# Optimization experiments

Measured on AMD Instinct MI355X. Metric: run time of the kernel, lower is better.

## Reference

```python
import jax, jax.numpy as jnp
import numpy as np

NSEG = 65  # instance ids live in [0, NSEG); must match setup_inputs fill_max
EPS = 1e-8


def setup_inputs() -> dict:
    key = jax.random.key(0)
    k1, k2 = jax.random.split(key)
    B, C, H, W = 8, 4, 1024, 1024
    logit = jax.random.normal(k1, (B, C, H, W), dtype=jnp.float32)
    inst_gt = jax.random.randint(k2, (B, H, W), 0, NSEG, dtype=jnp.int32)
    return {"logit": logit, "inst_gt": inst_gt}


def reference(logit, inst_gt):
    B, C, H, W = logit.shape
    N = H * W
    # softmax over channel dim (as F.softmax(logit, dim=1))
    p = jax.nn.softmax(logit, axis=1)                      # [B, C, H, W]
    p = p.reshape(B, C, N).transpose(0, 2, 1).reshape(B * N, C)  # [B*N, C]
    # one fused segment reduce over all batches: offset ids per batch element
    seg = (inst_gt.reshape(B, N) + jnp.arange(B, dtype=inst_gt.dtype)[:, None] * NSEG).reshape(-1)
    sums = jax.ops.segment_sum(p, seg, num_segments=B * NSEG)        # [B*NSEG, C]
    sumsq = jax.ops.segment_sum(p * p, seg, num_segments=B * NSEG)   # [B*NSEG, C]
    cnt = jax.ops.segment_sum(jnp.ones((B * N,), p.dtype), seg, num_segments=B * NSEG)  # [B*NSEG]
    cnt = cnt[:, None]                                               # [B*NSEG, 1]
    # unbiased variance per (batch, instance, channel): (sumsq - sum^2/n) / (n-1)
    n_safe = jnp.where(cnt > 0, cnt, 1.0)
    denom = jnp.where(cnt > 1, cnt - 1.0, 1.0)
    var = (sumsq - sums * sums / n_safe) / denom                     # [B*NSEG, C]
    var = var.reshape(B, NSEG, C)
    cnt = cnt.reshape(B, NSEG, 1)
    nonzero_id = (jnp.arange(NSEG) != 0)[None, :, None]              # skip background id 0
    # only instances with more than 1 pixel contribute variance
    valid = nonzero_id & (cnt > 1.0)
    sum_var = jnp.sum(jnp.where(valid, var, 0.0), axis=(1, 2))       # [B]
    # len(inst_ids): number of distinct nonzero ids present in each image
    num_ids = jnp.sum(jnp.where(nonzero_id[..., 0] & (cnt[..., 0] > 0.0), 1.0, 0.0), axis=1)  # [B]
    loss = jnp.mean(sum_var / (num_ids + EPS))
    return loss
```

## Files before the change

### kernel.cpp

```cpp
#include <hip/hip_runtime.h>


typedef unsigned int  uint32_t_;
typedef unsigned short u16x2 __attribute__((ext_vector_type(2)));
typedef unsigned int   u32x4 __attribute__((ext_vector_type(4)));
typedef short          s16x8 __attribute__((ext_vector_type(8)));
typedef float          f32x4 __attribute__((ext_vector_type(4)));

constexpr int   B_    = 8;
constexpr int   SEGS  = 64;
constexpr int   VALS  = 5;
constexpr float EPS_  = 1e-8f;

constexpr int PLANE   = 528;
constexpr int NSLOT   = 11;
constexpr int WLDS    = NSLOT * PLANE;
constexpr int LDS_SZ  = (4 * WLDS > 16384) ? 4 * WLDS : 16384;

__device__ __forceinline__ unsigned asu(float f)  { return __float_as_uint(f); }
__device__ __forceinline__ float    asf(unsigned u){ return __uint_as_float(u); }

__global__ __launch_bounds__(256) void vl_accum(const float* __restrict__ logit,
                                                const int*   __restrict__ inst,
                                                float* __restrict__ acc,
                                                int N, int ppb)
{
    __shared__ __align__(16) unsigned char lds[LDS_SZ];

    const int tid  = threadIdx.x;
    const int wid  = tid >> 6;
    const int lane = tid & 63;
    const int col  = lane & 15;
    const int quad = lane >> 4;
    const int wbase = wid * WLDS;

    *(uint2*)(lds + wbase + 8 * PLANE + lane * 8) = make_uint2(0x3F803F80u, 0x3F803F80u);
    *(uint2*)(lds + wbase + 9 * PLANE + lane * 8) = make_uint2(0u, 0u);

    int pl;
    if      (col < 4)              pl = col;
    else if (col >= 8 && col < 12) pl = col - 4;
    else if (col == 4)             pl = 8;
    else                           pl = 9;
    const int bRd   = wbase + pl * PLANE + quad * 16;
    const int segRd = wbase + 10 * PLANE + quad * 16;
    const int segWr = wbase + 10 * PLANE + lane * 8;

    u16x2 rowdup[4];
#pragma unroll
    for (int t = 0; t < 4; ++t) {
        unsigned short rw = (unsigned short)(t * 16 + col);
        rowdup[t] = (u16x2){rw, rw};
    }
    const u16x2 one2  = (u16x2){1, 1};
    const u16x2 bf1p  = (u16x2){0x3F80, 0x3F80};

    const int b = blockIdx.y;
    const float* __restrict__ l0 = logit + (size_t)b * 4 * N;
    const int*   __restrict__ ib = inst  + (size_t)b * N;

    f32x4 acc0 = {0.f,0.f,0.f,0.f}, acc1 = {0.f,0.f,0.f,0.f};
    f32x4 acc2 = {0.f,0.f,0.f,0.f}, acc3 = {0.f,0.f,0.f,0.f};

    const int blockStart = blockIdx.x * ppb;
    const int rounds = ppb >> 10;

    for (int r = 0; r < rounds; ++r) {
        const int q  = blockStart + (r << 10) + (wid << 8) + (lane << 2);
        const bool ok = (q + 4 <= N);
        const int qc = ok ? q : 0;

        float4 x0 = *(const float4*)(l0 + qc);
        float4 x1 = *(const float4*)(l0 + (size_t)N     + qc);
        float4 x2 = *(const float4*)(l0 + (size_t)2 * N + qc);
        float4 x3 = *(const float4*)(l0 + (size_t)3 * N + qc);
        int4   sg = *(const int4*)(ib + qc);
        if (!ok) sg = make_int4(0, 0, 0, 0);

        const float c0[4] = {x0.x, x0.y, x0.z, x0.w};
        const float c1[4] = {x1.x, x1.y, x1.z, x1.w};
        const float c2[4] = {x2.x, x2.y, x2.z, x2.w};
        const float c3[4] = {x3.x, x3.y, x3.z, x3.w};

        float P0[4], P1[4], P2[4], QQ[4];
#pragma unroll
        for (int i = 0; i < 4; ++i) {
            float va = c0[i], vb = c1[i], vc = c2[i], vd = c3[i];
            float m  = fmaxf(fmaxf(va, vb), fmaxf(vc, vd));
            float e0 = __expf(va - m);
            float e1 = __expf(vb - m);
            float e2 = __expf(vc - m);
            float e3 = __expf(vd - m);
            float rr = 1.0f / (e0 + e1 + e2 + e3);
            float q0 = e0 * rr, q1 = e1 * rr, q2 = e2 * rr, q3 = e3 * rr;
            P0[i] = q0; P1[i] = q1; P2[i] = q2;
            QQ[i] = q0*q0 + q1*q1 + q2*q2 + q3*q3;
        }

#define STAGE_PLANE(P, ARR)                                                     \
        {                                                                       \
            unsigned a0 = asu(ARR[0]), a1 = asu(ARR[1]);                        \
            unsigned a2 = asu(ARR[2]), a3 = asu(ARR[3]);                        \
            unsigned h1m = a1 & 0xFFFF0000u, h3m = a3 & 0xFFFF0000u;            \
            unsigned hi01 = (a0 >> 16) | h1m;                                   \
            unsigned hi23 = (a2 >> 16) | h3m;                                   \
            float l0f = ARR[0] - asf(a0 & 0xFFFF0000u);                         \
            float l1f = ARR[1] - asf(h1m);                                      \
            float l2f = ARR[2] - asf(a2 & 0xFFFF0000u);                         \
            float l3f = ARR[3] - asf(h3m);                                      \
            unsigned lo01 = (asu(l0f) >> 16) | (asu(l1f) & 0xFFFF0000u);        \
            unsigned lo23 = (asu(l2f) >> 16) | (asu(l3f) & 0xFFFF0000u);        \
            *(uint2*)(lds + wbase + (P) * PLANE + lane * 8)     = make_uint2(hi01, hi23); \
            *(uint2*)(lds + wbase + ((P)+4) * PLANE + lane * 8) = make_uint2(lo01, lo23); \
        }
        STAGE_PLANE(0, P0)
        STAGE_PLANE(1, P1)
        STAGE_PLANE(2, P2)
        STAGE_PLANE(3, QQ)
#undef STAGE_PLANE

        {
            unsigned r0 = (unsigned)(sg.x - 1) & 0xFFFFu;
            unsigned r1 = (unsigned)(sg.y - 1) & 0xFFFFu;
            unsigned r2 = (unsigned)(sg.z - 1) & 0xFFFFu;
            unsigned r3 = (unsigned)(sg.w - 1) & 0xFFFFu;
            *(uint2*)(lds + segWr) = make_uint2(r0 | (r1 << 16), r2 | (r3 << 16));
        }

#pragma unroll
        for (int kt = 0; kt < 8; ++kt) {
            s16x8 bfrag = *(const s16x8*)(lds + bRd   + kt * 64);
            u32x4 sv    = *(const u32x4*)(lds + segRd + kt * 64);

#define DO_TILE(T, ACC)                                                         \
            {                                                                   \
                u32x4 fr;                                                       \
                _Pragma("unroll")                                               \
                for (int i = 0; i < 4; ++i) {                                   \
                    u16x2 sp  = __builtin_bit_cast(u16x2, sv[i]);               \
                    u16x2 d   = sp - rowdup[T];                                 \
                    u16x2 mn  = __builtin_elementwise_min(d, one2);             \
                    u16x2 inv = one2 - mn;                                      \
                    u16x2 f   = inv * bf1p;                                     \
                    fr[i] = __builtin_bit_cast(unsigned, f);                    \
                }                                                               \
                s16x8 afrag = __builtin_bit_cast(s16x8, fr);                    \
                ACC = __builtin_amdgcn_mfma_f32_16x16x32_bf16(afrag, bfrag, ACC, 0, 0, 0); \
            }
            DO_TILE(0, acc0)
            DO_TILE(1, acc1)
            DO_TILE(2, acc2)
            DO_TILE(3, acc3)
#undef DO_TILE
        }
    }

    __syncthreads();
    float* cl = (float*)lds;
    {
        const int base = ((wid * 4) * 64 + lane) * 4;
        *(f32x4*)(cl + base)            = acc0;
        *(f32x4*)(cl + base + 64 * 4)   = acc1;
        *(f32x4*)(cl + base + 128 * 4)  = acc2;
        *(f32x4*)(cl + base + 192 * 4)  = acc3;
    }
    __syncthreads();

    for (int i = tid; i < SEGS * VALS; i += 256) {
        const int row = i / VALS;
        const int cc  = i - row * VALS;
        const int t   = row >> 4;
        const int rr  = row & 15;
        const int g   = rr >> 2;
        const int reg = rr & 3;
        const int lhi = g * 16 + cc;
        const int llo = lhi + 8;
        float v = 0.0f;
#pragma unroll
        for (int w = 0; w < 4; ++w) {
            v += cl[((w * 4 + t) * 64 + lhi) * 4 + reg];
            v += cl[((w * 4 + t) * 64 + llo) * 4 + reg];
        }
        unsafeAtomicAdd(acc + ((size_t)blockIdx.y * SEGS + row) * VALS + cc, v);
    }
}

__global__ __launch_bounds__(256) void vl_finalize(const float* __restrict__ acc,
                                                   float* __restrict__ out)
{
    __shared__ float sum_var[B_];
    __shared__ float num_ids[B_];
    if (threadIdx.x < B_) { sum_var[threadIdx.x] = 0.0f; num_ids[threadIdx.x] = 0.0f; }
    __syncthreads();

    for (int i = threadIdx.x; i < B_ * SEGS; i += 256) {
        const float* a = acc + (size_t)i * VALS;
        const int b = i >> 6;
        const float cnt = a[4];
        if (cnt > 1.0f) {
            const float inv_n = 1.0f / cnt;
            const float denom = cnt - 1.0f;
            const float s0 = a[0], s1 = a[1], s2 = a[2];
            const float s3 = cnt - s0 - s1 - s2;
            const float ssum2 = s0*s0 + s1*s1 + s2*s2 + s3*s3;
            const float sv = (a[3] - ssum2 * inv_n) / denom;
            atomicAdd(&sum_var[b], sv);
        }
        if (cnt > 0.0f) atomicAdd(&num_ids[b], 1.0f);
    }
    __syncthreads();

    if (threadIdx.x == 0) {
        float loss = 0.0f;
#pragma unroll
        for (int b = 0; b < B_; ++b) loss += sum_var[b] / (num_ids[b] + EPS_);
        out[0] = loss / (float)B_;
    }
}

extern "C" void kernel_launch(void* const* d_in, const int* in_sizes, int n_in,
                              void* d_out, int out_size, void* d_ws, size_t ws_size,
                              hipStream_t stream) {
    const float* logit = (const float*)d_in[0];
    const int*   inst  = (const int*)d_in[1];
    float* out = (float*)d_out;
    float* acc = (float*)d_ws;

    const int totalPix = in_sizes[1];
    const int N = totalPix / B_;

    hipMemsetAsync(acc, 0, (size_t)B_ * SEGS * VALS * sizeof(float), stream);

    const int gridx = 128;
    int ppb = (N + gridx - 1) / gridx;
    ppb = (ppb + 1023) & ~1023;

    dim3 grid(gridx, B_);
    vl_accum<<<grid, 256, 0, stream>>>(logit, inst, acc, N, ppb);
    vl_finalize<<<1, 256, 0, stream>>>(acc, out);
}
```

Baseline: 220.9 us.

## Prefetch next round's loads into registers and double the block grid

The main loop now issues the global loads for round r+1 before computing softmax, staging and MFMA for round r. This software-pipelines the loads so memory latency is hidden behind compute. The grid also doubles from 128 to 256 blocks per batch, which halves the pixels per block and adds more blocks to hide latency. The cost is higher register pressure from the prefetched values and more atomic accumulations at the end.

```diff
diff --git a/kernel.cpp b/kernel.cpp
--- a/kernel.cpp
+++ b/kernel.cpp
@@ -1,7 +1,6 @@
 #include <hip/hip_runtime.h>
 
 
-typedef unsigned int  uint32_t_;
 typedef unsigned short u16x2 __attribute__((ext_vector_type(2)));
 typedef unsigned int   u32x4 __attribute__((ext_vector_type(4)));
 typedef short          s16x8 __attribute__((ext_vector_type(8)));
@@ -64,23 +63,32 @@
 
     const int blockStart = blockIdx.x * ppb;
     const int rounds = ppb >> 10;
+    const int base0  = blockStart + (wid << 8) + (lane << 2);
+
+#define LOAD_ROUND(R, X0, X1, X2, X3, SG)                                       \
+    {                                                                           \
+        const int q  = base0 + ((R) << 10);                                     \
+        const bool ok = (q + 4 <= N);                                           \
+        const int qc = ok ? q : 0;                                              \
+        X0 = *(const float4*)(l0 + qc);                                         \
+        X1 = *(const float4*)(l0 + (size_t)N     + qc);                         \
+        X2 = *(const float4*)(l0 + (size_t)2 * N + qc);                         \
+        X3 = *(const float4*)(l0 + (size_t)3 * N + qc);                         \
+        int4 sgt = *(const int4*)(ib + qc);                                     \
+        SG = ok ? sgt : make_int4(0, 0, 0, 0);                                  \
+    }
+
+    float4 cx0, cx1, cx2, cx3; int4 csg;
+    if (rounds > 0) LOAD_ROUND(0, cx0, cx1, cx2, cx3, csg)
 
     for (int r = 0; r < rounds; ++r) {
-        const int q  = blockStart + (r << 10) + (wid << 8) + (lane << 2);
-        const bool ok = (q + 4 <= N);
-        const int qc = ok ? q : 0;
-
-        float4 x0 = *(const float4*)(l0 + qc);
-        float4 x1 = *(const float4*)(l0 + (size_t)N     + qc);
-        float4 x2 = *(const float4*)(l0 + (size_t)2 * N + qc);
-        float4 x3 = *(const float4*)(l0 + (size_t)3 * N + qc);
-        int4   sg = *(const int4*)(ib + qc);
-        if (!ok) sg = make_int4(0, 0, 0, 0);
-
-        const float c0[4] = {x0.x, x0.y, x0.z, x0.w};
-        const float c1[4] = {x1.x, x1.y, x1.z, x1.w};
-        const float c2[4] = {x2.x, x2.y, x2.z, x2.w};
-        const float c3[4] = {x3.x, x3.y, x3.z, x3.w};
+        float4 nx0, nx1, nx2, nx3; int4 nsg;
+        if (r + 1 < rounds) LOAD_ROUND(r + 1, nx0, nx1, nx2, nx3, nsg)
+
+        const float c0[4] = {cx0.x, cx0.y, cx0.z, cx0.w};
+        const float c1[4] = {cx1.x, cx1.y, cx1.z, cx1.w};
+        const float c2[4] = {cx2.x, cx2.y, cx2.z, cx2.w};
+        const float c3[4] = {cx3.x, cx3.y, cx3.z, cx3.w};
 
         float P0[4], P1[4], P2[4], QQ[4];
 #pragma unroll
@@ -120,10 +128,10 @@
 #undef STAGE_PLANE
 
         {
-            unsigned r0 = (unsigned)(sg.x - 1) & 0xFFFFu;
-            unsigned r1 = (unsigned)(sg.y - 1) & 0xFFFFu;
-            unsigned r2 = (unsigned)(sg.z - 1) & 0xFFFFu;
-            unsigned r3 = (unsigned)(sg.w - 1) & 0xFFFFu;
+            unsigned r0 = (unsigned)(csg.x - 1) & 0xFFFFu;
+            unsigned r1 = (unsigned)(csg.y - 1) & 0xFFFFu;
+            unsigned r2 = (unsigned)(csg.z - 1) & 0xFFFFu;
+            unsigned r3 = (unsigned)(csg.w - 1) & 0xFFFFu;
             *(uint2*)(lds + segWr) = make_uint2(r0 | (r1 << 16), r2 | (r3 << 16));
         }
 
@@ -153,7 +161,10 @@
             DO_TILE(3, acc3)
 #undef DO_TILE
         }
-    }
+
+        cx0 = nx0; cx1 = nx1; cx2 = nx2; cx3 = nx3; csg = nsg;
+    }
+#undef LOAD_ROUND
 
     __syncthreads();
     float* cl = (float*)lds;
@@ -231,7 +242,7 @@
 
     hipMemsetAsync(acc, 0, (size_t)B_ * SEGS * VALS * sizeof(float), stream);
 
-    const int gridx = 128;
+    const int gridx = 256;
     int ppb = (N + gridx - 1) / gridx;
     ppb = (ppb + 1023) & ~1023;
 
```

Result: no change. 223.0 us (+1.0%).

## Launch one 1024-pixel block per grid cell and split MFMA accumulator chains

Applied to the files above, without the earlier changes.

The persistent loop over rounds is removed and the grid now has one block per 1024 pixels (1024 blocks per image instead of 128), so each block processes a single round. The constant ones and zeros B planes are generated in registers via a per-lane select instead of being kept in LDS, which cuts LDS use from 11 to 9 planes per wave. MFMA accumulators are split into even and odd kt chains to shorten the dependency chain, and the one-hot build uses a multiply-add. The cost is many more blocks, each paying a full epilogue of LDS reduction plus 320 global atomics, so atomic traffic rises about eightfold.

```diff
diff --git a/kernel.cpp b/kernel.cpp
--- a/kernel.cpp
+++ b/kernel.cpp
@@ -1,7 +1,6 @@
 #include <hip/hip_runtime.h>
 
 
-typedef unsigned int  uint32_t_;
 typedef unsigned short u16x2 __attribute__((ext_vector_type(2)));
 typedef unsigned int   u32x4 __attribute__((ext_vector_type(4)));
 typedef short          s16x8 __attribute__((ext_vector_type(8)));
@@ -13,7 +12,7 @@
 constexpr float EPS_  = 1e-8f;
 
 constexpr int PLANE   = 528;
-constexpr int NSLOT   = 11;
+constexpr int NSLOT   = 9;
 constexpr int WLDS    = NSLOT * PLANE;
 constexpr int LDS_SZ  = (4 * WLDS > 16384) ? 4 * WLDS : 16384;
 
@@ -22,8 +21,8 @@
 
 __global__ __launch_bounds__(256) void vl_accum(const float* __restrict__ logit,
                                                 const int*   __restrict__ inst,
-                                                float* __restrict__ acc,
-                                                int N, int ppb)
+                                                float* __restrict__ accOut,
+                                                int N)
 {
     __shared__ __align__(16) unsigned char lds[LDS_SZ];
 
@@ -34,17 +33,13 @@
     const int quad = lane >> 4;
     const int wbase = wid * WLDS;
 
-    *(uint2*)(lds + wbase + 8 * PLANE + lane * 8) = make_uint2(0x3F803F80u, 0x3F803F80u);
-    *(uint2*)(lds + wbase + 9 * PLANE + lane * 8) = make_uint2(0u, 0u);
-
-    int pl;
-    if      (col < 4)              pl = col;
-    else if (col >= 8 && col < 12) pl = col - 4;
-    else if (col == 4)             pl = 8;
-    else                           pl = 9;
+    const bool selLds = (col < 4) | (col >= 8 && col < 12);
+    const unsigned cword = (col == 4) ? 0x3F803F80u : 0u;
+    const int pl = (col < 4) ? (2 * col)
+                 : ((col >= 8 && col < 12) ? (2 * (col - 8) + 1) : 0);
     const int bRd   = wbase + pl * PLANE + quad * 16;
-    const int segRd = wbase + 10 * PLANE + quad * 16;
-    const int segWr = wbase + 10 * PLANE + lane * 8;
+    const int segRd = wbase + 8 * PLANE + quad * 16;
+    const int segWr = wbase + 8 * PLANE + lane * 8;
 
     u16x2 rowdup[4];
 #pragma unroll
@@ -53,107 +48,112 @@
         rowdup[t] = (u16x2){rw, rw};
     }
     const u16x2 one2  = (u16x2){1, 1};
-    const u16x2 bf1p  = (u16x2){0x3F80, 0x3F80};
+    const u16x2 negb  = (u16x2){0xC080, 0xC080};
+    const u16x2 posb  = (u16x2){0x3F80, 0x3F80};
 
     const int b = blockIdx.y;
     const float* __restrict__ l0 = logit + (size_t)b * 4 * N;
     const int*   __restrict__ ib = inst  + (size_t)b * N;
 
-    f32x4 acc0 = {0.f,0.f,0.f,0.f}, acc1 = {0.f,0.f,0.f,0.f};
-    f32x4 acc2 = {0.f,0.f,0.f,0.f}, acc3 = {0.f,0.f,0.f,0.f};
-
-    const int blockStart = blockIdx.x * ppb;
-    const int rounds = ppb >> 10;
-
-    for (int r = 0; r < rounds; ++r) {
-        const int q  = blockStart + (r << 10) + (wid << 8) + (lane << 2);
-        const bool ok = (q + 4 <= N);
-        const int qc = ok ? q : 0;
-
-        float4 x0 = *(const float4*)(l0 + qc);
-        float4 x1 = *(const float4*)(l0 + (size_t)N     + qc);
-        float4 x2 = *(const float4*)(l0 + (size_t)2 * N + qc);
-        float4 x3 = *(const float4*)(l0 + (size_t)3 * N + qc);
-        int4   sg = *(const int4*)(ib + qc);
-        if (!ok) sg = make_int4(0, 0, 0, 0);
-
-        const float c0[4] = {x0.x, x0.y, x0.z, x0.w};
-        const float c1[4] = {x1.x, x1.y, x1.z, x1.w};
-        const float c2[4] = {x2.x, x2.y, x2.z, x2.w};
-        const float c3[4] = {x3.x, x3.y, x3.z, x3.w};
-
-        float P0[4], P1[4], P2[4], QQ[4];
-#pragma unroll
-        for (int i = 0; i < 4; ++i) {
-            float va = c0[i], vb = c1[i], vc = c2[i], vd = c3[i];
-            float m  = fmaxf(fmaxf(va, vb), fmaxf(vc, vd));
-            float e0 = __expf(va - m);
-            float e1 = __expf(vb - m);
-            float e2 = __expf(vc - m);
-            float e3 = __expf(vd - m);
-            float rr = 1.0f / (e0 + e1 + e2 + e3);
-            float q0 = e0 * rr, q1 = e1 * rr, q2 = e2 * rr, q3 = e3 * rr;
-            P0[i] = q0; P1[i] = q1; P2[i] = q2;
-            QQ[i] = q0*q0 + q1*q1 + q2*q2 + q3*q3;
-        }
+    const int q  = (blockIdx.x << 10) + (tid << 2);
+    const bool ok = (q + 4 <= N);
+    const int qc = ok ? q : 0;
+
+    float4 x0 = *(const float4*)(l0 + qc);
+    float4 x1 = *(const float4*)(l0 + (size_t)N     + qc);
+    float4 x2 = *(const float4*)(l0 + (size_t)2 * N + qc);
+    float4 x3 = *(const float4*)(l0 + (size_t)3 * N + qc);
+    int4   sg = *(const int4*)(ib + qc);
+    if (!ok) sg = make_int4(0, 0, 0, 0);
+
+    const float c0[4] = {x0.x, x0.y, x0.z, x0.w};
+    const float c1[4] = {x1.x, x1.y, x1.z, x1.w};
+    const float c2[4] = {x2.x, x2.y, x2.z, x2.w};
+    const float c3[4] = {x3.x, x3.y, x3.z, x3.w};
+
+    float P0[4], P1[4], P2[4], QQ[4];
+#pragma unroll
+    for (int i = 0; i < 4; ++i) {
+        float va = c0[i], vb = c1[i], vc = c2[i], vd = c3[i];
+        float m  = fmaxf(fmaxf(va, vb), fmaxf(vc, vd));
+        float e0 = __expf(va - m);
+        float e1 = __expf(vb - m);
+        float e2 = __expf(vc - m);
+        float e3 = __expf(vd - m);
+        float rr = 1.0f / (e0 + e1 + e2 + e3);
+        float q0 = e0 * rr, q1 = e1 * rr, q2 = e2 * rr, q3 = e3 * rr;
+        P0[i] = q0; P1[i] = q1; P2[i] = q2;
+        QQ[i] = q0*q0 + q1*q1 + q2*q2 + q3*q3;
+    }
 
 #define STAGE_PLANE(P, ARR)                                                     \
+    {                                                                           \
+        unsigned a0 = asu(ARR[0]), a1 = asu(ARR[1]);                            \
+        unsigned a2 = asu(ARR[2]), a3 = asu(ARR[3]);                            \
+        unsigned h1m = a1 & 0xFFFF0000u, h3m = a3 & 0xFFFF0000u;                \
+        unsigned hi01 = (a0 >> 16) | h1m;                                       \
+        unsigned hi23 = (a2 >> 16) | h3m;                                       \
+        float l0f = ARR[0] - asf(a0 & 0xFFFF0000u);                             \
+        float l1f = ARR[1] - asf(h1m);                                          \
+        float l2f = ARR[2] - asf(a2 & 0xFFFF0000u);                             \
+        float l3f = ARR[3] - asf(h3m);                                          \
+        unsigned lo01 = (asu(l0f) >> 16) | (asu(l1f) & 0xFFFF0000u);            \
+        unsigned lo23 = (asu(l2f) >> 16) | (asu(l3f) & 0xFFFF0000u);            \
+        *(uint2*)(lds + wbase + (2*(P)) * PLANE + lane * 8)   = make_uint2(hi01, hi23); \
+        *(uint2*)(lds + wbase + (2*(P)+1) * PLANE + lane * 8) = make_uint2(lo01, lo23); \
+    }
+    STAGE_PLANE(0, P0)
+    STAGE_PLANE(1, P1)
+    STAGE_PLANE(2, P2)
+    STAGE_PLANE(3, QQ)
+#undef STAGE_PLANE
+
+    {
+        unsigned r0 = (unsigned)(sg.x - 1) & 0xFFFFu;
+        unsigned r1 = (unsigned)(sg.y - 1) & 0xFFFFu;
+        unsigned r2 = (unsigned)(sg.z - 1) & 0xFFFFu;
+        unsigned r3 = (unsigned)(sg.w - 1) & 0xFFFFu;
+        *(uint2*)(lds + segWr) = make_uint2(r0 | (r1 << 16), r2 | (r3 << 16));
+    }
+
+    f32x4 acc0a = {0,0,0,0}, acc1a = {0,0,0,0}, acc2a = {0,0,0,0}, acc3a = {0,0,0,0};
+    f32x4 acc0b = {0,0,0,0}, acc1b = {0,0,0,0}, acc2b = {0,0,0,0}, acc3b = {0,0,0,0};
+
+#pragma unroll
+    for (int kt = 0; kt < 8; ++kt) {
+        s16x8 braw = *(const s16x8*)(lds + bRd   + kt * 64);
+        u32x4 sv   = *(const u32x4*)(lds + segRd + kt * 64);
+        u32x4 bw   = __builtin_bit_cast(u32x4, braw);
+#pragma unroll
+        for (int i = 0; i < 4; ++i) bw[i] = selLds ? bw[i] : cword;
+        s16x8 bfrag = __builtin_bit_cast(s16x8, bw);
+
+#define DO_TILE(T, ACC)                                                         \
         {                                                                       \
-            unsigned a0 = asu(ARR[0]), a1 = asu(ARR[1]);                        \
-            unsigned a2 = asu(ARR[2]), a3 = asu(ARR[3]);                        \
-            unsigned h1m = a1 & 0xFFFF0000u, h3m = a3 & 0xFFFF0000u;            \
-            unsigned hi01 = (a0 >> 16) | h1m;                                   \
-            unsigned hi23 = (a2 >> 16) | h3m;                                   \
-            float l0f = ARR[0] - asf(a0 & 0xFFFF0000u);                         \
-            float l1f = ARR[1] - asf(h1m);                                      \
-            float l2f = ARR[2] - asf(a2 & 0xFFFF0000u);                         \
-            float l3f = ARR[3] - asf(h3m);                                      \
-            unsigned lo01 = (asu(l0f) >> 16) | (asu(l1f) & 0xFFFF0000u);        \
-            unsigned lo23 = (asu(l2f) >> 16) | (asu(l3f) & 0xFFFF0000u);        \
-            *(uint2*)(lds + wbase + (P) * PLANE + lane * 8)     = make_uint2(hi01, hi23); \
-            *(uint2*)(lds + wbase + ((P)+4) * PLANE + lane * 8) = make_uint2(lo01, lo23); \
-        }
-        STAGE_PLANE(0, P0)
-        STAGE_PLANE(1, P1)
-        STAGE_PLANE(2, P2)
-        STAGE_PLANE(3, QQ)
-#undef STAGE_PLANE
-
-        {
-            unsigned r0 = (unsigned)(sg.x - 1) & 0xFFFFu;
-            unsigned r1 = (unsigned)(sg.y - 1) & 0xFFFFu;
-            unsigned r2 = (unsigned)(sg.z - 1) & 0xFFFFu;
-            unsigned r3 = (unsigned)(sg.w - 1) & 0xFFFFu;
-            *(uint2*)(lds + segWr) = make_uint2(r0 | (r1 << 16), r2 | (r3 << 16));
-        }
-
-#pragma unroll
-        for (int kt = 0; kt < 8; ++kt) {
-            s16x8 bfrag = *(const s16x8*)(lds + bRd   + kt * 64);
-            u32x4 sv    = *(const u32x4*)(lds + segRd + kt * 64);
-
-#define DO_TILE(T, ACC)                                                         \
-            {                                                                   \
-                u32x4 fr;                                                       \
-                _Pragma("unroll")                                               \
-                for (int i = 0; i < 4; ++i) {                                   \
-                    u16x2 sp  = __builtin_bit_cast(u16x2, sv[i]);               \
-                    u16x2 d   = sp - rowdup[T];                                 \
-                    u16x2 mn  = __builtin_elementwise_min(d, one2);             \
-                    u16x2 inv = one2 - mn;                                      \
-                    u16x2 f   = inv * bf1p;                                     \
-                    fr[i] = __builtin_bit_cast(unsigned, f);                    \
-                }                                                               \
-                s16x8 afrag = __builtin_bit_cast(s16x8, fr);                    \
-                ACC = __builtin_amdgcn_mfma_f32_16x16x32_bf16(afrag, bfrag, ACC, 0, 0, 0); \
-            }
-            DO_TILE(0, acc0)
-            DO_TILE(1, acc1)
-            DO_TILE(2, acc2)
-            DO_TILE(3, acc3)
+            u32x4 fr;                                                           \
+            _Pragma("unroll")                                                   \
+            for (int i = 0; i < 4; ++i) {                                       \
+                u16x2 sp  = __builtin_bit_cast(u16x2, sv[i]);                   \
+                u16x2 d   = sp - rowdup[T];                                     \
+                u16x2 mn  = __builtin_elementwise_min(d, one2);                 \
+                u16x2 f   = mn * negb + posb;                  \
+                fr[i] = __builtin_bit_cast(unsigned, f);                        \
+            }                                                                   \
+            s16x8 afrag = __builtin_bit_cast(s16x8, fr);                        \
+            ACC = __builtin_amdgcn_mfma_f32_16x16x32_bf16(afrag, bfrag, ACC, 0, 0, 0); \
+        }
+        if ((kt & 1) == 0) {
+            DO_TILE(0, acc0a) DO_TILE(1, acc1a) DO_TILE(2, acc2a) DO_TILE(3, acc3a)
+        } else {
+            DO_TILE(0, acc0b) DO_TILE(1, acc1b) DO_TILE(2, acc2b) DO_TILE(3, acc3b)
+        }
 #undef DO_TILE
-        }
-    }
+    }
+
+    f32x4 acc0 = acc0a + acc0b;
+    f32x4 acc1 = acc1a + acc1b;
+    f32x4 acc2 = acc2a + acc2b;
+    f32x4 acc3 = acc3a + acc3b;
 
     __syncthreads();
     float* cl = (float*)lds;
@@ -181,7 +181,7 @@
             v += cl[((w * 4 + t) * 64 + lhi) * 4 + reg];
             v += cl[((w * 4 + t) * 64 + llo) * 4 + reg];
         }
-        unsafeAtomicAdd(acc + ((size_t)blockIdx.y * SEGS + row) * VALS + cc, v);
+        unsafeAtomicAdd(accOut + ((size_t)blockIdx.y * SEGS + row) * VALS + cc, v);
     }
 }
 
@@ -231,11 +231,8 @@
 
     hipMemsetAsync(acc, 0, (size_t)B_ * SEGS * VALS * sizeof(float), stream);
 
-    const int gridx = 128;
-    int ppb = (N + gridx - 1) / gridx;
-    ppb = (ppb + 1023) & ~1023;
-
+    const int gridx = (N + 1023) >> 10;
     dim3 grid(gridx, B_);
-    vl_accum<<<grid, 256, 0, stream>>>(logit, inst, acc, N, ppb);
+    vl_accum<<<grid, 256, 0, stream>>>(logit, inst, acc, N);
     vl_finalize<<<1, 256, 0, stream>>>(acc, out);
 }
```

Result: slower. 236.4 us (+7.0%).
